# Kernel optimization log

Hardware: AMD Instinct MI355X
Metric: run time of the kernel (lower is better)

The kernel has to match this reference:

```python
import math
import jax, jax.numpy as jnp
import numpy as np

B, N_IN, C_IN = 32, 16384, 64
IMG = 128            # sqrt(N_IN)
E_BR = 64            # embed_dim per PRM branch
DILATIONS = (1, 2, 3)
DIM = E_BR * len(DILATIONS)   # 192, attn input dim
EMB = 64             # token_dims * head_cnt
M_FEAT = int(EMB * 0.5)       # 32 performer random features
EPS = 1e-8


def setup_inputs() -> dict:
    key = jax.random.key(0)
    ks = jax.random.split(key, 12)
    x = jax.random.normal(ks[0], (B, N_IN, C_IN), jnp.float32)
    # PRM: one conv per dilation, weights stacked [nb, O, I, kh, kw] (OIHW)
    conv_w = jax.random.normal(ks[1], (len(DILATIONS), E_BR, C_IN, 3, 3), jnp.float32) * 0.05
    conv_b = jax.random.normal(ks[2], (len(DILATIONS), E_BR), jnp.float32) * 0.01
    ln1_g = jnp.ones((DIM,), jnp.float32)
    ln1_b = jnp.zeros((DIM,), jnp.float32)
    kqv_w = jax.random.normal(ks[3], (DIM, 3 * EMB), jnp.float32) * 0.02
    kqv_b = jnp.zeros((3 * EMB,), jnp.float32)
    proj_w = jax.random.normal(ks[4], (EMB, EMB), jnp.float32) * 0.02
    proj_b = jnp.zeros((EMB,), jnp.float32)
    # performer random-feature matrix: orthogonal rows, scaled by sqrt(m) (non-trainable)
    rng = np.random.default_rng(0)
    q, _ = np.linalg.qr(rng.standard_normal((EMB, M_FEAT)))
    w_perf = jnp.asarray(q.T * math.sqrt(M_FEAT), jnp.float32)  # [m, emb]
    ln2_g = jnp.ones((EMB,), jnp.float32)
    ln2_b = jnp.zeros((EMB,), jnp.float32)
    mlp_w1 = jax.random.normal(ks[5], (EMB, EMB), jnp.float32) * 0.02
    mlp_b1 = jnp.zeros((EMB,), jnp.float32)
    mlp_w2 = jax.random.normal(ks[6], (EMB, EMB), jnp.float32) * 0.02
    mlp_b2 = jnp.zeros((EMB,), jnp.float32)
    return dict(x=x, conv_w=conv_w, conv_b=conv_b, ln1_g=ln1_g, ln1_b=ln1_b,
                kqv_w=kqv_w, kqv_b=kqv_b, proj_w=proj_w, proj_b=proj_b,
                w_perf=w_perf, ln2_g=ln2_g, ln2_b=ln2_b,
                mlp_w1=mlp_w1, mlp_b1=mlp_b1, mlp_w2=mlp_w2, mlp_b2=mlp_b2)


def _layernorm(x, g, b):
    mu = jnp.mean(x, axis=-1, keepdims=True)
    var = jnp.var(x, axis=-1, keepdims=True)
    return (x - mu) * jax.lax.rsqrt(var + 1e-5) * g + b


def _prm_exp(t, w):
    # t: [B, T, emb], w: [m, emb] -> exp(w.t - |t|^2/2) / sqrt(m)
    xd = 0.5 * jnp.sum(t * t, axis=-1, keepdims=True)       # [B, T, 1]
    wtx = jnp.einsum('btd,md->btm', t, w)                    # [B, T, m]
    return jnp.exp(wtx - xd) / math.sqrt(w.shape[0])


def reference(x, conv_w, conv_b, ln1_g, ln1_b, kqv_w, kqv_b, proj_w, proj_b,
              w_perf, ln2_g, ln2_b, mlp_w1, mlp_b1, mlp_w2, mlp_b2):
    Bx, N, C = x.shape
    # x.permute(0,2,1) then reshape to image NCHW
    img = jnp.transpose(x, (0, 2, 1)).reshape(Bx, C, IMG, IMG)
    # PRM: multi-dilation strided convs + GELU, channel-concat (branch-major)
    ys = []
    for i, d in enumerate(DILATIONS):
        pad = d  # ceil(((k-1)*d + 1 - stride)/2) for k=3, stride=2
        y = jax.lax.conv_general_dilated(
            img, conv_w[i], window_strides=(2, 2),
            padding=[(pad, pad), (pad, pad)], rhs_dilation=(d, d),
            dimension_numbers=('NCHW', 'OIHW', 'NCHW'))
        y = y + conv_b[i][None, :, None, None]
        ys.append(jax.nn.gelu(y, approximate=False))
    y = jnp.concatenate(ys, axis=1)                          # [B, 3*E, H', W']
    tokens = jnp.transpose(y.reshape(Bx, DIM, -1), (0, 2, 1))  # [B, T, 192]

    # Token_performer.attn on norm1(tokens)
    h = _layernorm(tokens, ln1_g, ln1_b)
    kqv = h @ kqv_w + kqv_b                                  # [B, T, 3*emb]
    k, q, v = jnp.split(kqv, 3, axis=-1)                     # split order: k, q, v
    kp = _prm_exp(k, w_perf)                                 # [B, T, m]
    qp = _prm_exp(q, w_perf)                                 # [B, T, m]
    D = jnp.einsum('btm,bm->bt', qp, jnp.sum(kp, axis=1))[..., None]   # [B, T, 1]
    kptv = jnp.einsum('btd,btm->bdm', v, kp)                 # [B, emb, m]
    yatt = jnp.einsum('btm,bdm->btd', qp, kptv) / (D + EPS)  # [B, T, emb]
    yatt = v + (yatt @ proj_w + proj_b)                      # skip inside single_attn (dropout=id at eval)

    # x = x + drop_path(mlp(norm2(x))) ; drop_path/dropout = identity at eval
    h2 = _layernorm(yatt, ln2_g, ln2_b)
    h2 = jax.nn.gelu(h2 @ mlp_w1 + mlp_b1, approximate=False) @ mlp_w2 + mlp_b2
    return yatt + h2
```

## Files before the change

kernel.cpp:

```cpp
#include <hip/hip_runtime.h>
#include <hip/hip_bf16.h>


#define TOK 4096
#define NB  32

typedef __attribute__((ext_vector_type(8)))  short short8;
typedef __attribute__((ext_vector_type(4)))  short short4v;
typedef __attribute__((ext_vector_type(16))) float f32x16;

__device__ __forceinline__ float gelu_fast(float v) {
    float u = v * fmaf(0.0713548162f, v * v, 1.5957691216f);
    float e = __expf(-u);
    return v * __builtin_amdgcn_rcpf(1.f + e);
}

__device__ __forceinline__ short f2bf(float f) {
    __hip_bfloat16 h = __float2bfloat16(f);
    return *reinterpret_cast<short*>(&h);
}

__device__ __forceinline__ float bf2f(short s) {
    union { unsigned u; float f; } x;
    x.u = ((unsigned)(unsigned short)s) << 16;
    return x.f;
}

__global__ __launch_bounds__(256) void k_prep(
        const float* __restrict__ cw, const float* __restrict__ kw,
        const float* __restrict__ pw, const float* __restrict__ w1,
        const float* __restrict__ w2m, const float* __restrict__ wperf,
        short* __restrict__ w2c, short* __restrict__ kwbf,
        short* __restrict__ pTbf, short* __restrict__ w1bf,
        short* __restrict__ w2bf, short* __restrict__ wpbf) {
    int idx = blockIdx.x * 256 + threadIdx.x;
    if (idx < 110592) {
        int c = idx & 63;
        int t = idx >> 6;
        int e = t & 63;
        int tap = t >> 6;
        int kwi = tap % 3, t2 = tap / 3;
        int r = t2 % 3, brr = t2 / 3;
        float v = cw[(((brr * 64 + e) * 64 + c) * 3 + r) * 3 + kwi];
        int dst = ((((brr * 9 + r * 3 + kwi) * 4 + (c >> 4)) * 2 + ((c >> 3) & 1)) * 64 + e) * 8 + (c & 7);
        w2c[dst] = f2bf(v);
    } else if (idx < 147456) {
        int i2 = idx - 110592;
        int o = i2 / 192, i = i2 % 192;
        int dst = (((i >> 4) * 2 + ((i >> 3) & 1)) * 192 + o) * 8 + (i & 7);
        kwbf[dst] = f2bf(kw[i * 192 + o]);
    } else if (idx < 151552) {
        int i2 = idx - 147456;
        int o = i2 >> 6, d = i2 & 63;
        int dst = (((d >> 4) * 2 + ((d >> 3) & 1)) * 64 + o) * 8 + (d & 7);
        pTbf[dst] = f2bf(pw[d * 64 + o]);
    } else if (idx < 155648) {
        int i2 = idx - 151552;
        int i = i2 >> 6, jd = i2 & 63;
        int dst = (((jd >> 4) * 2 + ((jd >> 3) & 1)) * 64 + i) * 8 + (jd & 7);
        w1bf[dst] = f2bf(w1[jd * 64 + i]);
    } else if (idx < 159744) {
        int i2 = idx - 155648;
        int o = i2 >> 6, i = i2 & 63;
        int dst = (((i >> 4) * 2 + ((i >> 3) & 1)) * 64 + o) * 8 + (i & 7);
        w2bf[dst] = f2bf(w2m[i * 64 + o]);
    } else if (idx < 161792) {
        int i2 = idx - 159744;
        int m = i2 >> 6, d = i2 & 63;
        int dst = (((d >> 4) * 2 + ((d >> 3) & 1)) * 32 + m) * 8 + (d & 7);
        wpbf[dst] = f2bf(wperf[m * 64 + d]);
    }
}

__global__ __launch_bounds__(256) void k_conv6(
        const float* __restrict__ x, const short* __restrict__ w2c,
        const float* __restrict__ cb, short* __restrict__ tokens) {
    const int wg  = blockIdx.x;
    const int swz_id = (wg & 7) * 768 + (wg >> 3);
    const int b   = swz_id / 192;
    const int rem = swz_id - b * 192;
    const int oh  = rem / 3;
    const int br  = rem - oh * 3;
    const int d   = br + 1;
    const int tid = threadIdx.x;
    const int lane = tid & 63;
    const int wv = tid >> 6;
    const int cl = lane & 31;
    const int g  = lane >> 5;
    const int wm = wv & 1;
    const int wn = wv >> 1;

    __shared__ short sA[3 * 68 * 2 * 32];

    const int ow = wm * 32 + cl;
    const int ecol = wn * 32 + cl;
    const short* wbr = w2c + br * 9 * 4096;

    f32x16 acc = {0.f, 0.f, 0.f, 0.f, 0.f, 0.f, 0.f, 0.f,
                  0.f, 0.f, 0.f, 0.f, 0.f, 0.f, 0.f, 0.f};

    for (int h = 0; h < 2; ++h) {
        if (h == 0 && tid < 96) {
            int s16 = tid & 7;
            int ii  = (tid >> 3) & 3;
            int r   = tid >> 5;
            int i   = (ii < 2) ? ii : (64 + ii);
            short8 z = {0, 0, 0, 0, 0, 0, 0, 0};
            *(short8*)((char*)sA + (r * 68 + i) * 128 + s16 * 16) = z;
        }
        for (int it = 0; it < 6; ++it) {
            int flat = it * 256 + tid;
            int c8l = flat & 3;
            int iw  = (flat >> 2) & 127;
            int r   = flat >> 9;
            int ih  = 2 * oh + (r - 1) * d;
            int iw4 = iw + 4;
            int i   = iw4 >> 1;
            int p   = iw4 & 1;
            char* dst = (char*)sA + (r * 68 + i) * 128
                      + ((((p * 4 + c8l) * 16)) ^ ((i & 7) << 4));
            if ((unsigned)ih < 128u) {
                const float* src = x + ((size_t)(b * 16384 + ih * 128 + iw)) * 64
                                 + h * 32 + c8l * 8;
                float4 f0 = *(const float4*)(src);
                float4 f1 = *(const float4*)(src + 4);
                short8 v;
                v[0] = f2bf(f0.x); v[1] = f2bf(f0.y); v[2] = f2bf(f0.z); v[3] = f2bf(f0.w);
                v[4] = f2bf(f1.x); v[5] = f2bf(f1.y); v[6] = f2bf(f1.z); v[7] = f2bf(f1.w);
                *(short8*)dst = v;
            } else {
                short8 z = {0, 0, 0, 0, 0, 0, 0, 0};
                *(short8*)dst = z;
            }
        }
        __syncthreads();

#pragma unroll
        for (int r = 0; r < 3; ++r) {
#pragma unroll
            for (int kwi = 0; kwi < 3; ++kwi) {
                const int iw4 = 2 * ow + (kwi - 1) * d + 4;
                const int i   = iw4 >> 1;
                const int p   = iw4 & 1;
                const char* arow = (const char*)sA + (r * 68 + i) * 128;
                const int swzk = (i & 7) << 4;
                const short* wt = wbr + (r * 3 + kwi) * 4096;
#pragma unroll
                for (int kk = 0; kk < 2; ++kk) {
                    const int ks = h * 2 + kk;
                    short8 a = *(const short8*)(arow + ((((p * 4 + kk * 2 + g) * 16)) ^ swzk));
                    short8 bf = *(const short8*)(wt + ((ks * 2 + g) * 64 + ecol) * 8);
                    acc = __builtin_amdgcn_mfma_f32_32x32x16_bf16(a, bf, acc, 0, 0, 0);
                }
            }
        }
        __syncthreads();
    }

    {
        const int eG = br * 64 + wn * 32 + cl;
        const float bias = cb[eG];
#pragma unroll
        for (int reg = 0; reg < 16; ++reg) {
            int owl = wm * 32 + (reg & 3) + 8 * (reg >> 2) + 4 * g;
            sA[owl * 66 + wn * 32 + cl] = f2bf(gelu_fast(acc[reg] + bias));
        }
    }
    __syncthreads();
    {
        const int tr = tid >> 2, c16 = tid & 3;
        short8 v0 = *(const short8*)(sA + tr * 66 + c16 * 16);
        short8 v1 = *(const short8*)(sA + tr * 66 + c16 * 16 + 8);
        short* ob = tokens + ((size_t)(b * TOK + oh * 64 + tr)) * 192
                  + br * 64 + c16 * 16;
        *(short8*)(ob) = v0;
        *(short8*)(ob + 8) = v1;
    }
}

__global__ __launch_bounds__(256) void k_lnkqvp(
        const short* __restrict__ tokens, const float* __restrict__ g,
        const float* __restrict__ be, const short* __restrict__ wbf,
        const float* __restrict__ bias, const short* __restrict__ wpbf,
        short* __restrict__ vT, short* __restrict__ kpT,
        short* __restrict__ qpT) {
    const int b = blockIdx.y;
    const int t0 = blockIdx.x * 64;
    const int tid = threadIdx.x;

    __shared__ short sB[64 * 192];
    __shared__ float red[64 * 8];
    __shared__ float xdk[128];
    __shared__ float xdq[128];

    const int r = tid >> 2, q = tid & 3;
    const short* rowp = tokens + ((size_t)(b * TOK + t0 + r)) * 192 + q * 48;
    float v[48];
    float s1 = 0.f, s2 = 0.f;
#pragma unroll
    for (int i = 0; i < 6; ++i) {
        short8 x8 = *(const short8*)(rowp + i * 8);
#pragma unroll
        for (int j = 0; j < 8; ++j) {
            float f = bf2f(x8[j]);
            v[i * 8 + j] = f;
            s1 += f;
            s2 = fmaf(f, f, s2);
        }
    }
    red[r * 8 + q] = s1;
    red[r * 8 + 4 + q] = s2;
    __syncthreads();
    const float m1 = red[r * 8 + 0] + red[r * 8 + 1] + red[r * 8 + 2] + red[r * 8 + 3];
    const float m2 = red[r * 8 + 4] + red[r * 8 + 5] + red[r * 8 + 6] + red[r * 8 + 7];
    const float mu = m1 * (1.f / 192.f);
    const float var = m2 * (1.f / 192.f) - mu * mu;
    const float rs = rsqrtf(fmaxf(var, 0.f) + 1e-5f);
    const float4* g4 = (const float4*)(g + q * 48);
    const float4* b4 = (const float4*)(be + q * 48);
    char* rowB = (char*)sB + r * 384;
    const int swz = (r & 7) << 4;
#pragma unroll
    for (int i = 0; i < 12; ++i) {
        float4 gg = g4[i], bb = b4[i];
        short4v pk;
        pk.x = f2bf((v[4 * i + 0] - mu) * rs * gg.x + bb.x);
        pk.y = f2bf((v[4 * i + 1] - mu) * rs * gg.y + bb.y);
        pk.z = f2bf((v[4 * i + 2] - mu) * rs * gg.z + bb.z);
        pk.w = f2bf((v[4 * i + 3] - mu) * rs * gg.w + bb.w);
        *(short4v*)(rowB + (((q * 48 + i * 4) * 2) ^ swz)) = pk;
    }
    __syncthreads();

    const int lane = tid & 63;
    const int wv = tid >> 6;
    const int tt = wv & 1;
    const int wo = wv >> 1;
    const int colL = lane & 31;
    const int gq = lane >> 5;

    f32x16 acc0 = {0.f, 0.f, 0.f, 0.f, 0.f, 0.f, 0.f, 0.f,
                   0.f, 0.f, 0.f, 0.f, 0.f, 0.f, 0.f, 0.f};
    f32x16 acc1 = acc0, acc2 = acc0;
    const char* bbase = (const char*)sB + (tt * 32 + colL) * 384;
    const int bswz = ((tt * 32 + colL) & 7) << 4;
    const int ocol = wo * 32 + colL;

    for (int kk = 0; kk < 12; ++kk) {
        short8 bf = *(const short8*)(bbase + (((kk * 16 + gq * 8) * 2) ^ bswz));
        const short* ak = wbf + ((kk * 2 + gq) * 192 + ocol) * 8;
        short8 a0 = *(const short8*)(ak);
        short8 a1 = *(const short8*)(ak + 64 * 8);
        short8 a2 = *(const short8*)(ak + 128 * 8);
        acc0 = __builtin_amdgcn_mfma_f32_32x32x16_bf16(a0, bf, acc0, 0, 0, 0);
        acc1 = __builtin_amdgcn_mfma_f32_32x32x16_bf16(a1, bf, acc1, 0, 0, 0);
        acc2 = __builtin_amdgcn_mfma_f32_32x32x16_bf16(a2, bf, acc2, 0, 0, 0);
    }

    const int tl = tt * 32 + colL;
    const int tglob = t0 + tl;

    float kb[16], qb[16];
    float sk = 0.f, sq = 0.f;
    {
        short* vb = vT + (size_t)b * 64 * TOK + tglob;
#pragma unroll
        for (int reg = 0; reg < 16; ++reg) {
            int orow = (reg & 3) + 8 * (reg >> 2) + 4 * gq;
            int d = wo * 32 + orow;
            kb[reg] = acc0[reg] + bias[d];
            qb[reg] = acc1[reg] + bias[64 + d];
            float vv = acc2[reg] + bias[128 + d];
            vb[(size_t)d * TOK] = f2bf(vv);
            sk = fmaf(kb[reg], kb[reg], sk);
            sq = fmaf(qb[reg], qb[reg], sq);
        }
    }
    sk += __shfl_xor(sk, 32, 64);
    sq += __shfl_xor(sq, 32, 64);
    __syncthreads();

    if (gq == 0) {
        xdk[wo * 64 + tl] = 0.5f * sk;
        xdq[wo * 64 + tl] = 0.5f * sq;
    }
    {
        char* kS = (char*)sB;
        char* qS = (char*)sB + 8192;
        const int tswz = (tl & 7) << 4;
#pragma unroll
        for (int rq = 0; rq < 4; ++rq) {
            int d0 = wo * 32 + 8 * rq + 4 * gq;
            short4v pk, pq;
#pragma unroll
            for (int j = 0; j < 4; ++j) {
                ((short*)&pk)[j] = f2bf(kb[rq * 4 + j]);
                ((short*)&pq)[j] = f2bf(qb[rq * 4 + j]);
            }
            *(short4v*)(kS + tl * 128 + ((d0 * 2) ^ tswz)) = pk;
            *(short4v*)(qS + tl * 128 + ((d0 * 2) ^ tswz)) = pq;
        }
    }
    __syncthreads();

    {
        const int pass = wv >> 1;
        const int tt2 = wv & 1;
        const char* S = (char*)sB + pass * 8192;
        const int t2 = tt2 * 32 + colL;
        const int t2swz = (t2 & 7) << 4;
        f32x16 pacc = {0.f, 0.f, 0.f, 0.f, 0.f, 0.f, 0.f, 0.f,
                       0.f, 0.f, 0.f, 0.f, 0.f, 0.f, 0.f, 0.f};
#pragma unroll
        for (int ks = 0; ks < 4; ++ks) {
            short8 a = *(const short8*)(wpbf + ((ks * 2 + gq) * 32 + colL) * 8);
            short8 bb = *(const short8*)(S + t2 * 128 + (((ks * 16 + gq * 8) * 2) ^ t2swz));
            pacc = __builtin_amdgcn_mfma_f32_32x32x16_bf16(a, bb, pacc, 0, 0, 0);
        }
        const float* xda = pass ? xdq : xdk;
        const float xdv = xda[t2] + xda[64 + t2];
        short* dst = (pass ? qpT : kpT) + (size_t)b * 32 * TOK + t0 + t2;
#pragma unroll
        for (int reg = 0; reg < 16; ++reg) {
            int m = (reg & 3) + 8 * (reg >> 2) + 4 * gq;
            float kpv = __expf(pacc[reg] - xdv) * 0.17677669529663687f;
            dst[(size_t)m * TOK] = f2bf(kpv);
        }
    }
}

__global__ __launch_bounds__(256) void k_kptv(
        const short* __restrict__ vT, const short* __restrict__ kpT,
        float* __restrict__ kvp, float* __restrict__ skpp) {
    const int b = blockIdx.y, ch = blockIdx.x, tid = threadIdx.x;
    const int t = ch * 256 + tid;
    __shared__ float sv[256 * 65 + 256 * 36];
    float* skp = sv + 256 * 65;
    for (int dd = 0; dd < 64; ++dd)
        sv[tid * 65 + dd] = bf2f(vT[((size_t)(b * 64 + dd)) * TOK + t]);
    for (int m = 0; m < 32; ++m)
        skp[tid * 36 + m] = bf2f(kpT[((size_t)(b * 32 + m)) * TOK + t]);
    __syncthreads();

    const int dd = tid & 63;
    const int mg = __builtin_amdgcn_readfirstlane(tid >> 6);
    float acc[8];
#pragma unroll
    for (int j = 0; j < 8; ++j) acc[j] = 0.f;
    for (int tt = 0; tt < 256; ++tt) {
        float vv = sv[tt * 65 + dd];
        const float4* kq = (const float4*)(skp + tt * 36 + mg * 8);
        float4 a0 = kq[0], a1 = kq[1];
        acc[0] = fmaf(vv, a0.x, acc[0]);
        acc[1] = fmaf(vv, a0.y, acc[1]);
        acc[2] = fmaf(vv, a0.z, acc[2]);
        acc[3] = fmaf(vv, a0.w, acc[3]);
        acc[4] = fmaf(vv, a1.x, acc[4]);
        acc[5] = fmaf(vv, a1.y, acc[5]);
        acc[6] = fmaf(vv, a1.z, acc[6]);
        acc[7] = fmaf(vv, a1.w, acc[7]);
    }
    float* dst = kvp + (((size_t)(b * 16 + ch) * 64 + dd) * 32) + mg * 8;
#pragma unroll
    for (int j = 0; j < 8; ++j) dst[j] = acc[j];

    if (tid < 32) {
        float s = 0.f;
        for (int tt = 0; tt < 256; ++tt) s += skp[tt * 36 + tid];
        skpp[(b * 16 + ch) * 32 + tid] = s;
    }
}

__global__ __launch_bounds__(256) void k_reduce2(
        const float* __restrict__ kvp, const float* __restrict__ skpp,
        short* __restrict__ kvbf, float* __restrict__ sum_kp) {
    int idx = blockIdx.x * 256 + threadIdx.x;
    if (idx < 65536) {
        int b = idx >> 11, rem = idx & 2047, dd = rem >> 5, m = rem & 31;
        float s = 0.f;
        for (int ch = 0; ch < 16; ++ch) s += kvp[((b * 16 + ch) * 64 + dd) * 32 + m];
        int dst = (((b * 2 + (m >> 4)) * 2 + ((m >> 3) & 1)) * 64 + dd) * 8 + (m & 7);
        kvbf[dst] = f2bf(s);
    } else if (idx < 65536 + 1024) {
        int i = idx - 65536;
        int b = i >> 5, m = i & 31;
        float s = 0.f;
        for (int ch = 0; ch < 16; ++ch) s += skpp[(b * 16 + ch) * 32 + m];
        sum_kp[i] = s;
    }
}

__global__ __launch_bounds__(256) void k_fuse(
        const short* __restrict__ vT, const short* __restrict__ qpT,
        const short* __restrict__ kvbf, const float* __restrict__ sum_kp,
        const short* __restrict__ pTbf, const float* __restrict__ proj_b,
        const float* __restrict__ g2, const float* __restrict__ b2ln,
        const short* __restrict__ w1bf, const float* __restrict__ b1,
        const short* __restrict__ w2bf, const float* __restrict__ b2,
        float* __restrict__ out) {
    const int b = blockIdx.y;
    const int t0 = blockIdx.x * 64;
    const int tid = threadIdx.x;
    const int lane = tid & 63;
    const int cl = lane & 31;
    const int g  = lane >> 5;
    const int wv = tid >> 6;
    const int wr = wv & 1;
    const int wc = wv >> 1;

    __shared__ __align__(16) char pool[29952];
    short* qpS  = (short*)(pool + 0);
    short* ytS  = (short*)(pool + 5120);
    short* xnS  = (short*)(pool + 14336);
    short* hgS  = (short*)(pool + 0);
    float* outS = (float*)(pool + 9216);
    float* red  = (float*)(pool + 26624);
    float* stat = (float*)(pool + 27648);
    float* coefS= (float*)(pool + 28672);

    if (tid < 64) {
        coefS[tid]       = proj_b[tid];
        coefS[64 + tid]  = g2[tid];
        coefS[128 + tid] = b2ln[tid];
        coefS[192 + tid] = b1[tid];
        coefS[256 + tid] = b2[tid];
    }
    {
        const int t = tid & 63, q = tid >> 6;
        const float* sk = sum_kp + b * 32;
        float dsum = 0.f;
        short8 pk;
#pragma unroll
        for (int i = 0; i < 8; ++i) {
            int m = q * 8 + i;
            short s = qpT[((size_t)(b * 32 + m)) * TOK + t0 + t];
            dsum = fmaf(bf2f(s), sk[m], dsum);
            pk[i] = s;
        }
        *(short8*)(qpS + t * 40 + q * 8) = pk;
        red[t * 4 + q] = dsum;
    }
    __syncthreads();

    const int tl = wc * 32 + cl;
    const int tg = t0 + tl;
    const int rcol = wr * 32 + cl;

    f32x16 acc = {0.f, 0.f, 0.f, 0.f, 0.f, 0.f, 0.f, 0.f,
                  0.f, 0.f, 0.f, 0.f, 0.f, 0.f, 0.f, 0.f};
    {
        const short* Ab = kvbf + (size_t)b * 2048;
        short8 a0 = *(const short8*)(Ab + (g * 64 + rcol) * 8);
        short8 a1 = *(const short8*)(Ab + ((2 + g) * 64 + rcol) * 8);
        short8 b0 = *(const short8*)(qpS + tl * 40 + g * 8);
        short8 b1v = *(const short8*)(qpS + tl * 40 + 16 + g * 8);
        acc = __builtin_amdgcn_mfma_f32_32x32x16_bf16(a0, b0, acc, 0, 0, 0);
        acc = __builtin_amdgcn_mfma_f32_32x32x16_bf16(a1, b1v, acc, 0, 0, 0);
    }
    {
        float Dv = red[tl * 4 + 0] + red[tl * 4 + 1] + red[tl * 4 + 2] + red[tl * 4 + 3];
        float rD = 1.f / (Dv + 1e-8f);
#pragma unroll
        for (int rq = 0; rq < 4; ++rq) {
            int d0 = wr * 32 + 8 * rq + 4 * g;
            short4v p;
            p.x = f2bf(acc[rq * 4 + 0] * rD);
            p.y = f2bf(acc[rq * 4 + 1] * rD);
            p.z = f2bf(acc[rq * 4 + 2] * rD);
            p.w = f2bf(acc[rq * 4 + 3] * rD);
            *(short4v*)(ytS + tl * 72 + d0) = p;
        }
    }
    __syncthreads();

    f32x16 acc2 = {0.f, 0.f, 0.f, 0.f, 0.f, 0.f, 0.f, 0.f,
                   0.f, 0.f, 0.f, 0.f, 0.f, 0.f, 0.f, 0.f};
    {
#pragma unroll
        for (int ks = 0; ks < 4; ++ks) {
            short8 a = *(const short8*)(pTbf + ((ks * 2 + g) * 64 + rcol) * 8);
            short8 bb = *(const short8*)(ytS + tl * 72 + ks * 16 + g * 8);
            acc2 = __builtin_amdgcn_mfma_f32_32x32x16_bf16(a, bb, acc2, 0, 0, 0);
        }
    }
    float skv[16];
    {
        const short* vb = vT + (size_t)b * 64 * TOK + tg;
#pragma unroll
        for (int reg = 0; reg < 16; ++reg) {
            int o = wr * 32 + (reg & 3) + 8 * (reg >> 2) + 4 * g;
            skv[reg] = acc2[reg] + bf2f(vb[(size_t)o * TOK]) + coefS[o];
        }
    }

    {
        float s1 = 0.f, s2 = 0.f;
#pragma unroll
        for (int reg = 0; reg < 16; ++reg) {
            s1 += skv[reg];
            s2 = fmaf(skv[reg], skv[reg], s2);
        }
        s1 += __shfl_xor(s1, 32, 64);
        s2 += __shfl_xor(s2, 32, 64);
        if (g == 0) {
            stat[(wr * 64 + tl) * 2 + 0] = s1;
            stat[(wr * 64 + tl) * 2 + 1] = s2;
        }
        __syncthreads();
        float S1 = s1 + stat[((wr ^ 1) * 64 + tl) * 2 + 0];
        float S2 = s2 + stat[((wr ^ 1) * 64 + tl) * 2 + 1];
        float mu = S1 * (1.f / 64.f);
        float var = S2 * (1.f / 64.f) - mu * mu;
        float rs = rsqrtf(fmaxf(var, 0.f) + 1e-5f);
#pragma unroll
        for (int rq = 0; rq < 4; ++rq) {
            int o0 = wr * 32 + 8 * rq + 4 * g;
            short4v p;
#pragma unroll
            for (int j = 0; j < 4; ++j) {
                int o = o0 + j;
                float xn = (skv[rq * 4 + j] - mu) * rs * coefS[64 + o] + coefS[128 + o];
                ((short*)&p)[j] = f2bf(xn);
            }
            *(short4v*)(xnS + tl * 72 + o0) = p;
        }
    }
    __syncthreads();

    f32x16 acc3 = {0.f, 0.f, 0.f, 0.f, 0.f, 0.f, 0.f, 0.f,
                   0.f, 0.f, 0.f, 0.f, 0.f, 0.f, 0.f, 0.f};
    {
#pragma unroll
        for (int ks = 0; ks < 4; ++ks) {
            short8 a = *(const short8*)(w1bf + ((ks * 2 + g) * 64 + rcol) * 8);
            short8 bb = *(const short8*)(xnS + tl * 72 + ks * 16 + g * 8);
            acc3 = __builtin_amdgcn_mfma_f32_32x32x16_bf16(a, bb, acc3, 0, 0, 0);
        }
    }
    __syncthreads();
    {
#pragma unroll
        for (int rq = 0; rq < 4; ++rq) {
            int i0 = wr * 32 + 8 * rq + 4 * g;
            short4v p;
#pragma unroll
            for (int j = 0; j < 4; ++j) {
                int i = i0 + j;
                float hgv = gelu_fast(acc3[rq * 4 + j] + coefS[192 + i]);
                ((short*)&p)[j] = f2bf(hgv);
            }
            *(short4v*)(hgS + tl * 72 + i0) = p;
        }
    }
    __syncthreads();

    f32x16 acc4 = {0.f, 0.f, 0.f, 0.f, 0.f, 0.f, 0.f, 0.f,
                   0.f, 0.f, 0.f, 0.f, 0.f, 0.f, 0.f, 0.f};
    {
#pragma unroll
        for (int ks = 0; ks < 4; ++ks) {
            short8 a = *(const short8*)(w2bf + ((ks * 2 + g) * 64 + rcol) * 8);
            short8 bb = *(const short8*)(hgS + tl * 72 + ks * 16 + g * 8);
            acc4 = __builtin_amdgcn_mfma_f32_32x32x16_bf16(a, bb, acc4, 0, 0, 0);
        }
    }
    {
#pragma unroll
        for (int rq = 0; rq < 4; ++rq) {
            int o0 = wr * 32 + 8 * rq + 4 * g;
            float4 f;
#pragma unroll
            for (int j = 0; j < 4; ++j) {
                int o = o0 + j;
                ((float*)&f)[j] = skv[rq * 4 + j] + acc4[rq * 4 + j] + coefS[256 + o];
            }
            *(float4*)(outS + tl * 68 + o0) = f;
        }
    }
    __syncthreads();

    {
        const int tt = tid >> 2, qq = tid & 3;
        float* ob = out + ((size_t)(b * TOK) + t0 + tt) * 64;
#pragma unroll
        for (int it = 0; it < 4; ++it) {
            *(float4*)(ob + it * 16 + qq * 4) =
                *(float4*)(outS + tt * 68 + it * 16 + qq * 4);
        }
    }
}

extern "C" void kernel_launch(void* const* d_in, const int* in_sizes, int n_in,
                              void* d_out, int out_size, void* d_ws, size_t ws_size,
                              hipStream_t stream) {
    const float* x      = (const float*)d_in[0];
    const float* conv_w = (const float*)d_in[1];
    const float* conv_b = (const float*)d_in[2];
    const float* ln1_g  = (const float*)d_in[3];
    const float* ln1_b  = (const float*)d_in[4];
    const float* kqv_w  = (const float*)d_in[5];
    const float* kqv_b  = (const float*)d_in[6];
    const float* proj_w = (const float*)d_in[7];
    const float* proj_b = (const float*)d_in[8];
    const float* w_perf = (const float*)d_in[9];
    const float* ln2_g  = (const float*)d_in[10];
    const float* ln2_b  = (const float*)d_in[11];
    const float* mlp_w1 = (const float*)d_in[12];
    const float* mlp_b1 = (const float*)d_in[13];
    const float* mlp_w2 = (const float*)d_in[14];
    const float* mlp_b2 = (const float*)d_in[15];

    float* ws = (float*)d_ws;
    short* w2c    = (short*)ws;
    short* kwbf   = (short*)(ws + 55296);
    short* pTbf   = (short*)(ws + 73728);
    short* w1bf   = (short*)(ws + 75776);
    short* w2bf   = (short*)(ws + 77824);
    short* wpbf   = (short*)(ws + 79872);
    float* sum_kp = ws + 80896;
    short* kvbf   = (short*)(ws + 81920);
    short* tokens = (short*)(ws + 114688);
    float* wsB    = ws + 114688 + 12582912;
    short* vT     = (short*)wsB;
    short* qpT    = (short*)(wsB + 4194304);
    short* kpT    = (short*)(wsB + 6291456);
    float* skpp   = wsB + 8388608;
    float* kvp    = wsB + 8404992;
    float* outp   = (float*)d_out;

    k_prep   <<<632, 256, 0, stream>>>(conv_w, kqv_w, proj_w, mlp_w1, mlp_w2,
                                       w_perf, w2c, kwbf, pTbf, w1bf, w2bf, wpbf);
    k_conv6  <<<6144, 256, 0, stream>>>(x, w2c, conv_b, tokens);
    k_lnkqvp <<<dim3(64, 32), 256, 0, stream>>>(tokens, ln1_g, ln1_b, kwbf,
                                                kqv_b, wpbf, vT, kpT, qpT);
    k_kptv   <<<dim3(16, 32), 256, 0, stream>>>(vT, kpT, kvp, skpp);
    k_reduce2<<<260, 256, 0, stream>>>(kvp, skpp, kvbf, sum_kp);
    k_fuse   <<<dim3(64, 32), 256, 0, stream>>>(vT, qpT, kvbf, sum_kp,
                                                pTbf, proj_b, ln2_g, ln2_b,
                                                w1bf, mlp_b1, w2bf, mlp_b2, outp);
}
```

Measured before the change: 156.1 us.

## Split conv channel staging into four 16-channel phases to halve LDS

The conv kernel now stages the input-channel dimension in four phases of 16 channels instead of two of 32. This halves the shared-memory tile and uses a new XOR swizzle for the narrower 64-byte rows, so more workgroups can be resident per CU. The cost is twice as many load/sync phases. Each pixel is also fetched in 64-byte pieces across phases, which may hurt global-load efficiency and leave less overlap within each workgroup.

```diff
diff --git a/kernel.cpp b/kernel.cpp
--- a/kernel.cpp
+++ b/kernel.cpp
@@ -72,7 +72,7 @@
     }
 }
 
-__global__ __launch_bounds__(256) void k_conv6(
+__global__ __launch_bounds__(256) void k_conv9(
         const float* __restrict__ x, const short* __restrict__ w2c,
         const float* __restrict__ cb, short* __restrict__ tokens) {
     const int wg  = blockIdx.x;
@@ -90,7 +90,7 @@
     const int wm = wv & 1;
     const int wn = wv >> 1;
 
-    __shared__ short sA[3 * 68 * 2 * 32];
+    __shared__ short sA[3 * 68 * 32];
 
     const int ow = wm * 32 + cl;
     const int ecol = wn * 32 + cl;
@@ -99,29 +99,30 @@
     f32x16 acc = {0.f, 0.f, 0.f, 0.f, 0.f, 0.f, 0.f, 0.f,
                   0.f, 0.f, 0.f, 0.f, 0.f, 0.f, 0.f, 0.f};
 
-    for (int h = 0; h < 2; ++h) {
-        if (h == 0 && tid < 96) {
-            int s16 = tid & 7;
-            int ii  = (tid >> 3) & 3;
-            int r   = tid >> 5;
-            int i   = (ii < 2) ? ii : (64 + ii);
-            short8 z = {0, 0, 0, 0, 0, 0, 0, 0};
-            *(short8*)((char*)sA + (r * 68 + i) * 128 + s16 * 16) = z;
-        }
-        for (int it = 0; it < 6; ++it) {
+    if (tid < 48) {
+        int s  = tid & 3;
+        int ii = (tid >> 2) & 3;
+        int r  = tid >> 4;
+        int i  = (ii < 2) ? ii : (64 + ii);
+        short8 z = {0, 0, 0, 0, 0, 0, 0, 0};
+        *(short8*)((char*)sA + (r * 68 + i) * 64 + s * 16) = z;
+    }
+
+    for (int ph = 0; ph < 4; ++ph) {
+        for (int it = 0; it < 3; ++it) {
             int flat = it * 256 + tid;
-            int c8l = flat & 3;
-            int iw  = (flat >> 2) & 127;
-            int r   = flat >> 9;
+            int c8h = flat & 1;
+            int iw  = (flat >> 1) & 127;
+            int r   = flat >> 8;
             int ih  = 2 * oh + (r - 1) * d;
             int iw4 = iw + 4;
             int i   = iw4 >> 1;
             int p   = iw4 & 1;
-            char* dst = (char*)sA + (r * 68 + i) * 128
-                      + ((((p * 4 + c8l) * 16)) ^ ((i & 7) << 4));
+            char* dst = (char*)sA + (r * 68 + i) * 64
+                      + 16 * ((p * 2 + c8h) ^ ((i >> 1) & 3));
             if ((unsigned)ih < 128u) {
                 const float* src = x + ((size_t)(b * 16384 + ih * 128 + iw)) * 64
-                                 + h * 32 + c8l * 8;
+                                 + ph * 16 + c8h * 8;
                 float4 f0 = *(const float4*)(src);
                 float4 f1 = *(const float4*)(src + 4);
                 short8 v;
@@ -142,16 +143,11 @@
                 const int iw4 = 2 * ow + (kwi - 1) * d + 4;
                 const int i   = iw4 >> 1;
                 const int p   = iw4 & 1;
-                const char* arow = (const char*)sA + (r * 68 + i) * 128;
-                const int swzk = (i & 7) << 4;
-                const short* wt = wbr + (r * 3 + kwi) * 4096;
-#pragma unroll
-                for (int kk = 0; kk < 2; ++kk) {
-                    const int ks = h * 2 + kk;
-                    short8 a = *(const short8*)(arow + ((((p * 4 + kk * 2 + g) * 16)) ^ swzk));
-                    short8 bf = *(const short8*)(wt + ((ks * 2 + g) * 64 + ecol) * 8);
-                    acc = __builtin_amdgcn_mfma_f32_32x32x16_bf16(a, bf, acc, 0, 0, 0);
-                }
+                short8 a = *(const short8*)((char*)sA + (r * 68 + i) * 64
+                           + 16 * ((p * 2 + g) ^ ((i >> 1) & 3)));
+                short8 bf = *(const short8*)(wbr + (r * 3 + kwi) * 4096
+                           + ((ph * 2 + g) * 64 + ecol) * 8);
+                acc = __builtin_amdgcn_mfma_f32_32x32x16_bf16(a, bf, acc, 0, 0, 0);
             }
         }
         __syncthreads();
@@ -630,7 +626,7 @@
 
     k_prep   <<<632, 256, 0, stream>>>(conv_w, kqv_w, proj_w, mlp_w1, mlp_w2,
                                        w_perf, w2c, kwbf, pTbf, w1bf, w2bf, wpbf);
-    k_conv6  <<<6144, 256, 0, stream>>>(x, w2c, conv_b, tokens);
+    k_conv9  <<<6144, 256, 0, stream>>>(x, w2c, conv_b, tokens);
     k_lnkqvp <<<dim3(64, 32), 256, 0, stream>>>(tokens, ln1_g, ln1_b, kwbf,
                                                 kqv_b, wpbf, vT, kpT, qpT);
     k_kptv   <<<dim3(16, 32), 256, 0, stream>>>(vT, kpT, kvp, skpp);
```

Result: slower. 163.3 us (+4.6%).
